# Kernel tuning notes

Hardware: AMD Instinct MI355X
Metric: run time of the kernel (lower is better)

Reference implementation:

```python
import jax, jax.numpy as jnp
import numpy as np

CLASS_NUM = 80
NUM_PRED = 2
TOPK = 1000
LEVEL_SIZES = [147456, 36864, 9216, 2304, 576]


def _make_anchors(key, n):
    k1, k2, k3, k4 = jax.random.split(key, 4)
    x1 = jax.random.uniform(k1, (n,)) * 1000.0
    y1 = jax.random.uniform(k2, (n,)) * 1000.0
    w = jax.random.uniform(k3, (n,)) * 200.0 + 8.0
    h = jax.random.uniform(k4, (n,)) * 200.0 + 8.0
    return jnp.stack([x1, y1, x1 + w, y1 + h], axis=1)


def setup_inputs() -> dict:
    key = jax.random.key(0)
    inp = {}
    for i, n in enumerate(LEVEL_SIZES):
        ka = jax.random.fold_in(key, 3 * i)
        kc = jax.random.fold_in(key, 3 * i + 1)
        kr = jax.random.fold_in(key, 3 * i + 2)
        inp[f"anchors{i}"] = _make_anchors(ka, n)
        inp[f"cls{i}"] = jax.random.normal(kc, (1, n, CLASS_NUM * NUM_PRED), dtype=jnp.float32)
        inp[f"reg{i}"] = jax.random.normal(kr, (1, n, 4 * NUM_PRED), dtype=jnp.float32) * 0.1
    return inp


def bbox_transform_inv(anchors, deltas):
    # anchors: [N,4] (x1,y1,x2,y2); deltas: [N,4] (dx,dy,dw,dh)
    w = anchors[:, 2] - anchors[:, 0] + 1.0
    h = anchors[:, 3] - anchors[:, 1] + 1.0
    cx = anchors[:, 0] + 0.5 * w
    cy = anchors[:, 1] + 0.5 * h
    pcx = cx + deltas[:, 0] * w
    pcy = cy + deltas[:, 1] * h
    pw = w * jnp.exp(deltas[:, 2])
    ph = h * jnp.exp(deltas[:, 3])
    return jnp.stack([pcx - 0.5 * pw, pcy - 0.5 * ph,
                      pcx + 0.5 * pw, pcy + 0.5 * ph], axis=1)


def _per_layer_inference(anchors_list, cls_list, reg_list):
    keep_a, keep_c, keep_r = [], [], []
    for a, c, r in zip(anchors_list, cls_list, reg_list):
        a = a.reshape(-1, 4)
        c = c[0].reshape(-1, CLASS_NUM * NUM_PRED)
        r = r[0].reshape(-1, 4 * NUM_PRED)
        if a.shape[0] > TOPK:
            ruler = jnp.max(c, axis=1)
            _, inds = jax.lax.top_k(ruler, TOPK)
            a, c, r = a[inds], c[inds], r[inds]
        keep_a.append(a)
        keep_c.append(jax.nn.sigmoid(c))
        keep_r.append(r)
    a = jnp.concatenate(keep_a, axis=0)   # [N,4]
    c = jnp.concatenate(keep_c, axis=0)   # [N, C*P]
    r = jnp.concatenate(keep_r, axis=0)   # [N, 4*P]
    n = a.shape[0]
    tag = (jnp.arange(CLASS_NUM, dtype=a.dtype) + 1.0)
    tag = jnp.tile(tag[None, :], (n, 1)).reshape(-1, 1)  # [N*C,1]
    scores0 = c[:, :CLASS_NUM].reshape(-1, 1)
    scores1 = c[:, CLASS_NUM:].reshape(-1, 1)
    bbox0 = bbox_transform_inv(a, r[:, :4])
    bbox1 = bbox_transform_inv(a, r[:, 4:])
    bbox0 = jnp.tile(bbox0, (1, CLASS_NUM)).reshape(-1, 4)
    bbox1 = jnp.tile(bbox1, (1, CLASS_NUM)).reshape(-1, 4)
    pred0 = jnp.concatenate([bbox0, scores0, tag], axis=1)
    pred1 = jnp.concatenate([bbox1, scores1, tag], axis=1)
    return jnp.concatenate([pred0, pred1], axis=1)  # [N*C, 12]


def reference(anchors0, anchors1, anchors2, anchors3, anchors4,
              cls0, cls1, cls2, cls3, cls4,
              reg0, reg1, reg2, reg3, reg4):
    return _per_layer_inference(
        [anchors0, anchors1, anchors2, anchors3, anchors4],
        [cls0, cls1, cls2, cls3, cls4],
        [reg0, reg1, reg2, reg3, reg4])
```

## Files before the change

kernel.cpp:

```cpp
#include <hip/hip_runtime.h>

#define CLS   160
#define TOPKN 1000
#define N0 147456
#define N1 36864
#define N2 9216
#define N3 2304
#define N4 576
#define NROWS (N0 + N1 + N2 + N3)
#define BD1 N0
#define BD2 (N0 + N1)
#define BD3 (N0 + N1 + N2)
#define NSEL (4 * TOPKN + N4)
#define NBINS 65536
#define CAND_CAP 2048

__device__ __forceinline__ unsigned sortable(float f) {
    unsigned u = __float_as_uint(f);
    return (u & 0x80000000u) ? ~u : (u | 0x80000000u);
}

__global__ __launch_bounds__(256) void k_ruler(
    const float* __restrict__ c0, const float* __restrict__ c1,
    const float* __restrict__ c2, const float* __restrict__ c3,
    unsigned* __restrict__ keys, unsigned* __restrict__ hist)
{
    int tid = blockIdx.x * 256 + threadIdx.x;
    if (tid < 4 * NBINS + 4096 + 8) hist[tid] = 0;

    int r0 = blockIdx.x << 7;
    const float* cb; int lr0;
    if (r0 < BD1)      { cb = c0; lr0 = r0; }
    else if (r0 < BD2) { cb = c1; lr0 = r0 - BD1; }
    else if (r0 < BD3) { cb = c2; lr0 = r0 - BD2; }
    else               { cb = c3; lr0 = r0 - BD3; }

    int wv   = threadIdx.x >> 6;
    int lane = threadIdx.x & 63;
    int sub  = lane >> 3;
    int col  = lane & 7;
    #pragma unroll
    for (int i = 0; i < 4; ++i) {
        int rrel = wv * 32 + i * 8 + sub;
        const float4* p = (const float4*)cb + (size_t)(lr0 + rrel) * 40 + col;
        float m = -3.4e38f;
        #pragma unroll
        for (int k = 0; k < 5; ++k) {
            float4 v = p[8 * k];
            m = fmaxf(m, fmaxf(fmaxf(v.x, v.y), fmaxf(v.z, v.w)));
        }
        m = fmaxf(m, __shfl_xor(m, 1));
        m = fmaxf(m, __shfl_xor(m, 2));
        m = fmaxf(m, __shfl_xor(m, 4));
        if (col == 0) keys[r0 + rrel] = sortable(m);
    }
}

__global__ __launch_bounds__(256) void k_hist(const unsigned* __restrict__ keys,
                                              unsigned* __restrict__ hist,
                                              unsigned* __restrict__ coarse)
{
    int b        = blockIdx.x;
    int level    = b >> 8;
    unsigned seg = (b >> 4) & 15;
    int chunk    = b & 15;
    __shared__ unsigned cnt[4096];
    for (int i = threadIdx.x; i < 4096; i += 256) cnt[i] = 0;
    __syncthreads();
    int base, n;
    switch (level) {
        case 0:  base = 0;   n = N0; break;
        case 1:  base = BD1; n = N1; break;
        case 2:  base = BD2; n = N2; break;
        default: base = BD3; n = N3; break;
    }
    int q = n >> 4;
    const uint4* kp = (const uint4*)(keys + base + chunk * q);
    int nv = q >> 2;
    for (int i = threadIdx.x; i < nv; i += 256) {
        uint4 k = kp[i];
        unsigned b0 = k.x >> 16, b1 = k.y >> 16, b2 = k.z >> 16, b3 = k.w >> 16;
        if ((b0 >> 12) == seg) atomicAdd(&cnt[b0 & 4095u], 1u);
        if ((b1 >> 12) == seg) atomicAdd(&cnt[b1 & 4095u], 1u);
        if ((b2 >> 12) == seg) atomicAdd(&cnt[b2 & 4095u], 1u);
        if ((b3 >> 12) == seg) atomicAdd(&cnt[b3 & 4095u], 1u);
    }
    __syncthreads();
    unsigned* h = hist + level * NBINS + (seg << 12);
    for (int i = threadIdx.x; i < 4096; i += 256) {
        unsigned c = cnt[i];
        if (c) atomicAdd(&h[i], c);
    }
    if (threadIdx.x < 64) {
        int j = threadIdx.x;
        unsigned s2 = 0;
        #pragma unroll 8
        for (int i = 0; i < 64; ++i) s2 += cnt[j * 64 + ((i + j) & 63)];
        if (s2) atomicAdd(&coarse[level * 1024 + (int)(seg << 6) + j], s2);
    }
}

__global__ __launch_bounds__(1024) void k_compact(const unsigned* __restrict__ keys,
                                                  const unsigned* __restrict__ hist,
                                                  const unsigned* __restrict__ coarse,
                                                  unsigned* __restrict__ ctrl,
                                                  uint2* __restrict__ cand)
{
    int level = blockIdx.x >> 4;
    int slice = blockIdx.x & 15;
    int t     = threadIdx.x;
    int lane  = t & 63;

    __shared__ unsigned s[1024];
    __shared__ unsigned thr_s, chunk_s, cum0_s;

    s[t] = coarse[level * 1024 + t];
    __syncthreads();
    for (int off = 1; off < 1024; off <<= 1) {
        unsigned v   = s[t];
        unsigned add = (t + off < 1024) ? s[t + off] : 0u;
        __syncthreads();
        s[t] = v + add;
        __syncthreads();
    }
    if (s[t] >= TOPKN && (t == 1023 || s[t + 1] < TOPKN)) {
        chunk_s = (unsigned)t;
        cum0_s  = (t == 1023) ? 0u : s[t + 1];
    }
    __syncthreads();
    if (t < 64) {
        const unsigned* h = hist + level * NBINS;
        unsigned c = h[chunk_s * 64 + (unsigned)t];
        unsigned sufw = c;
        #pragma unroll
        for (int off = 1; off < 64; off <<= 1) {
            unsigned v = __shfl_down(sufw, off);
            if (t + off < 64) sufw += v;
        }
        unsigned long long mask = __ballot(cum0_s + sufw >= TOPKN);
        if (t == 0)
            thr_s = (chunk_s * 64 + (63 - (unsigned)__clzll(mask))) << 16;
    }
    __syncthreads();
    unsigned thr = thr_s;

    int base = (level == 0) ? 0 : (level == 1) ? BD1 : (level == 2) ? BD2 : BD3;
    int n    = (level == 0) ? N0 : (level == 1) ? N1 : (level == 2) ? N2 : N3;
    int ns = n >> 4;
    const uint4* kp = (const uint4*)(keys + base + slice * ns);
    int nv = ns >> 2;
    for (int i = t; i < nv; i += 1024) {
        uint4 k4 = kp[i];
        unsigned kv[4] = {k4.x, k4.y, k4.z, k4.w};
        #pragma unroll
        for (int c = 0; c < 4; ++c) {
            bool pass = kv[c] >= thr;
            unsigned long long mask = __ballot(pass);
            if (pass) {
                int leader    = __ffsll((long long)mask) - 1;
                unsigned tot  = (unsigned)__popcll(mask);
                unsigned rank = (unsigned)__popcll(mask & ((1ull << lane) - 1ull));
                unsigned bp = 0;
                if (lane == leader) bp = atomicAdd(&ctrl[4 + level], tot);
                bp = (unsigned)__shfl((int)bp, leader);
                unsigned pos = bp + rank;
                if (pos < CAND_CAP)
                    cand[level * CAND_CAP + pos] =
                        make_uint2(kv[c], (unsigned)(slice * ns + 4 * i + c));
            }
        }
    }
}

__global__ __launch_bounds__(1024) void k_rank(const uint2* __restrict__ cand,
                                               const unsigned* __restrict__ ctrl,
                                               unsigned* __restrict__ sel)
{
    int level = blockIdx.x;
    unsigned cnt = ctrl[4 + level];
    if (cnt > CAND_CAP) cnt = CAND_CAP;
    __shared__ unsigned long long a[CAND_CAP];
    for (int i = threadIdx.x; i < (int)cnt; i += 1024) {
        uint2 c = cand[level * CAND_CAP + i];
        a[i] = ((unsigned long long)c.x << 32) | (unsigned)(~c.y);
    }
    __syncthreads();
    for (int i = threadIdx.x; i < (int)cnt; i += 1024) {
        unsigned long long mine = a[i];
        unsigned rank = 0;
        for (int j = 0; j < (int)cnt; ++j) rank += (a[j] > mine) ? 1u : 0u;
        if (rank < TOPKN)
            sel[level * TOPKN + rank] = ~(unsigned)(mine & 0xFFFFFFFFull);
    }
}

__global__ __launch_bounds__(256) void k_epilogue(
    const float* a0, const float* a1, const float* a2, const float* a3, const float* a4,
    const float* c0, const float* c1, const float* c2, const float* c3, const float* c4,
    const float* r0, const float* r1, const float* r2, const float* r3, const float* r4,
    const unsigned* __restrict__ sel, float* __restrict__ out)
{
    int s = blockIdx.x;
    int level, idx;
    if (s < 4 * TOPKN) {
        level = s / TOPKN;
        idx   = (int)sel[s];
    } else {
        level = 4;
        idx   = s - 4 * TOPKN;
    }
    const float *A, *C, *R;
    switch (level) {
        case 0: A = a0; C = c0; R = r0; break;
        case 1: A = a1; C = c1; R = r1; break;
        case 2: A = a2; C = c2; R = r2; break;
        case 3: A = a3; C = c3; R = r3; break;
        default: A = a4; C = c4; R = r4; break;
    }

    __shared__ float sc[CLS];
    __shared__ float bb[8];

    const float* cp = C + (size_t)idx * CLS;
    if (threadIdx.x < CLS) {
        float x = cp[threadIdx.x];
        sc[threadIdx.x] = 1.0f / (1.0f + __expf(-x));
    }
    if (threadIdx.x == 192) {
        const float* ap = A + (size_t)idx * 4;
        const float* rp = R + (size_t)idx * 8;
        float x1 = ap[0], y1 = ap[1], x2 = ap[2], y2 = ap[3];
        float w  = x2 - x1 + 1.0f, h = y2 - y1 + 1.0f;
        float cx = x1 + 0.5f * w,  cy = y1 + 0.5f * h;
        #pragma unroll
        for (int p = 0; p < 2; ++p) {
            float pcx = cx + rp[4 * p + 0] * w;
            float pcy = cy + rp[4 * p + 1] * h;
            float pw  = w * __expf(rp[4 * p + 2]);
            float ph  = h * __expf(rp[4 * p + 3]);
            bb[4 * p + 0] = pcx - 0.5f * pw;
            bb[4 * p + 1] = pcy - 0.5f * ph;
            bb[4 * p + 2] = pcx + 0.5f * pw;
            bb[4 * p + 3] = pcy + 0.5f * ph;
        }
    }
    __syncthreads();

    float4* orow = (float4*)(out + (size_t)s * 960);
    if (threadIdx.x < 240) {
        int j = threadIdx.x / 3, part = threadIdx.x % 3;
        float tag = (float)(j + 1);
        float4 v;
        if (part == 0)      v = make_float4(bb[0], bb[1], bb[2], bb[3]);
        else if (part == 1) v = make_float4(sc[j], tag, bb[4], bb[5]);
        else                v = make_float4(bb[6], bb[7], sc[80 + j], tag);
        orow[threadIdx.x] = v;
    }
}

extern "C" void kernel_launch(void* const* d_in, const int* in_sizes, int n_in,
                              void* d_out, int out_size, void* d_ws, size_t ws_size,
                              hipStream_t stream)
{
    bool interleaved = (in_sizes[1] > 1000000);
    const float *A[5], *C[5], *R[5];
    for (int i = 0; i < 5; ++i) {
        if (interleaved) {
            A[i] = (const float*)d_in[3 * i + 0];
            C[i] = (const float*)d_in[3 * i + 1];
            R[i] = (const float*)d_in[3 * i + 2];
        } else {
            A[i] = (const float*)d_in[i];
            C[i] = (const float*)d_in[5 + i];
            R[i] = (const float*)d_in[10 + i];
        }
    }

    unsigned* keys   = (unsigned*)d_ws;
    unsigned* hist   = keys + NROWS;
    unsigned* coarse = hist + 4 * NBINS;
    unsigned* ctrl   = coarse + 4096;
    uint2*    cand   = (uint2*)(ctrl + 8);
    unsigned* sel    = (unsigned*)(cand + 4 * CAND_CAP);

    k_ruler<<<1530, 256, 0, stream>>>(C[0], C[1], C[2], C[3], keys, hist);
    k_hist<<<1024, 256, 0, stream>>>(keys, hist, coarse);
    k_compact<<<64, 1024, 0, stream>>>(keys, hist, coarse, ctrl, cand);
    k_rank<<<4, 1024, 0, stream>>>(cand, ctrl, sel);
    k_epilogue<<<NSEL, 256, 0, stream>>>(A[0], A[1], A[2], A[3], A[4],
                                         C[0], C[1], C[2], C[3], C[4],
                                         R[0], R[1], R[2], R[3], R[4],
                                         sel, (float*)d_out);
}
```

Measured before the change: 90.08 us.

## Split threshold decision from compaction and spread compaction across many blocks

The per-level threshold search (prefix scan over coarse and fine histograms) moves into its own small kernel that stores the threshold in a control word. Compaction becomes a separate one-key-per-thread kernel over all rows, launched with many more blocks. The goal is to stop every slice block from repeating the scan and to raise parallelism for the filter pass. The cost is an extra kernel launch and a global round-trip for the threshold.

```diff
diff --git a/kernel.cpp b/kernel.cpp
--- a/kernel.cpp
+++ b/kernel.cpp
@@ -100,19 +100,14 @@
     }
 }
 
-__global__ __launch_bounds__(1024) void k_compact(const unsigned* __restrict__ keys,
-                                                  const unsigned* __restrict__ hist,
-                                                  const unsigned* __restrict__ coarse,
-                                                  unsigned* __restrict__ ctrl,
-                                                  uint2* __restrict__ cand)
-{
-    int level = blockIdx.x >> 4;
-    int slice = blockIdx.x & 15;
+__global__ __launch_bounds__(1024) void k_decide(const unsigned* __restrict__ hist,
+                                                 const unsigned* __restrict__ coarse,
+                                                 unsigned* __restrict__ ctrl)
+{
+    int level = blockIdx.x;
     int t     = threadIdx.x;
-    int lane  = t & 63;
-
     __shared__ unsigned s[1024];
-    __shared__ unsigned thr_s, chunk_s, cum0_s;
+    __shared__ unsigned chunk_s, cum0_s;
 
     s[t] = coarse[level * 1024 + t];
     __syncthreads();
@@ -131,44 +126,42 @@
     if (t < 64) {
         const unsigned* h = hist + level * NBINS;
         unsigned c = h[chunk_s * 64 + (unsigned)t];
-        unsigned sufw = c;
+        unsigned suf = c;
         #pragma unroll
         for (int off = 1; off < 64; off <<= 1) {
-            unsigned v = __shfl_down(sufw, off);
-            if (t + off < 64) sufw += v;
-        }
-        unsigned long long mask = __ballot(cum0_s + sufw >= TOPKN);
+            unsigned v = __shfl_down(suf, off);
+            if (t + off < 64) suf += v;
+        }
+        unsigned long long mask = __ballot(cum0_s + suf >= TOPKN);
         if (t == 0)
-            thr_s = (chunk_s * 64 + (63 - (unsigned)__clzll(mask))) << 16;
-    }
-    __syncthreads();
-    unsigned thr = thr_s;
-
-    int base = (level == 0) ? 0 : (level == 1) ? BD1 : (level == 2) ? BD2 : BD3;
-    int n    = (level == 0) ? N0 : (level == 1) ? N1 : (level == 2) ? N2 : N3;
-    int ns = n >> 4;
-    const uint4* kp = (const uint4*)(keys + base + slice * ns);
-    int nv = ns >> 2;
-    for (int i = t; i < nv; i += 1024) {
-        uint4 k4 = kp[i];
-        unsigned kv[4] = {k4.x, k4.y, k4.z, k4.w};
-        #pragma unroll
-        for (int c = 0; c < 4; ++c) {
-            bool pass = kv[c] >= thr;
-            unsigned long long mask = __ballot(pass);
-            if (pass) {
-                int leader    = __ffsll((long long)mask) - 1;
-                unsigned tot  = (unsigned)__popcll(mask);
-                unsigned rank = (unsigned)__popcll(mask & ((1ull << lane) - 1ull));
-                unsigned bp = 0;
-                if (lane == leader) bp = atomicAdd(&ctrl[4 + level], tot);
-                bp = (unsigned)__shfl((int)bp, leader);
-                unsigned pos = bp + rank;
-                if (pos < CAND_CAP)
-                    cand[level * CAND_CAP + pos] =
-                        make_uint2(kv[c], (unsigned)(slice * ns + 4 * i + c));
-            }
-        }
+            ctrl[level] = ((chunk_s << 6) + (63u - (unsigned)__clzll(mask))) << 16;
+    }
+}
+
+__global__ __launch_bounds__(256) void k_compact(const unsigned* __restrict__ keys,
+                                                 unsigned* __restrict__ ctrl,
+                                                 uint2* __restrict__ cand)
+{
+    int w = blockIdx.x * 256 + threadIdx.x;
+    int lane = threadIdx.x & 63;
+    int level, base;
+    if (w < BD1)      { level = 0; base = 0;   }
+    else if (w < BD2) { level = 1; base = BD1; }
+    else if (w < BD3) { level = 2; base = BD2; }
+    else              { level = 3; base = BD3; }
+    unsigned key = keys[w];
+    bool pass = key >= ctrl[level];
+    unsigned long long mask = __ballot(pass);
+    if (pass) {
+        int leader    = __ffsll((long long)mask) - 1;
+        unsigned tot  = (unsigned)__popcll(mask);
+        unsigned rank = (unsigned)__popcll(mask & ((1ull << lane) - 1ull));
+        unsigned bpos = 0;
+        if (lane == leader) bpos = atomicAdd(&ctrl[4 + level], tot);
+        bpos = (unsigned)__shfl((int)bpos, leader);
+        unsigned pos = bpos + rank;
+        if (pos < CAND_CAP)
+            cand[level * CAND_CAP + pos] = make_uint2(key, (unsigned)(w - base));
     }
 }
 
@@ -285,7 +278,8 @@
 
     k_ruler<<<1530, 256, 0, stream>>>(C[0], C[1], C[2], C[3], keys, hist);
     k_hist<<<1024, 256, 0, stream>>>(keys, hist, coarse);
-    k_compact<<<64, 1024, 0, stream>>>(keys, hist, coarse, ctrl, cand);
+    k_decide<<<4, 1024, 0, stream>>>(hist, coarse, ctrl);
+    k_compact<<<NROWS / 256, 256, 0, stream>>>(keys, ctrl, cand);
     k_rank<<<4, 1024, 0, stream>>>(cand, ctrl, sel);
     k_epilogue<<<NSEL, 256, 0, stream>>>(A[0], A[1], A[2], A[3], A[4],
                                          C[0], C[1], C[2], C[3], C[4],
```

Result: no change. 90.06 us (-0.0%).
